# Kernel tuning notes

Measured on AMD Instinct MI355X. Metric: run time of the kernel, lower is better.

Reference implementation:

```python
import jax, jax.numpy as jnp
import numpy as np

N_E = 4096
E_DIM = 64
BETA = 0.25


def setup_inputs() -> dict:
    key = jax.random.key(0)
    k1, k2 = jax.random.split(key)
    z = jax.random.normal(k1, (16, E_DIM, 32, 32), dtype=jnp.float32)
    embedding = jax.random.normal(k2, (N_E, E_DIM), dtype=jnp.float32)
    return {"z": z, "embedding": embedding}


def reference(z, embedding):
    # b c h w -> b h w c
    zc = jnp.transpose(z, (0, 2, 3, 1))  # [B,H,W,C]
    B, H, W, C = zc.shape
    zf = zc.reshape(-1, C)  # [N, C]

    # Squared Euclidean distances (argmin is identical to cdist p=2 argmin)
    # d2[n,e] = |z|^2 - 2 z.e + |e|^2
    d2 = (
        jnp.sum(zf * zf, axis=1, keepdims=True)
        - 2.0 * (zf @ embedding.T)
        + jnp.sum(embedding * embedding, axis=1)[None, :]
    )  # [N, n_e]
    idx = jnp.argmin(d2, axis=1)  # [N]

    z_q = embedding[idx].reshape(B, H, W, C)

    # dist_p == 2 losses
    loss_d1 = jnp.mean((jax.lax.stop_gradient(z_q) - zc) ** 2)
    loss_d2 = jnp.mean((z_q - jax.lax.stop_gradient(zc)) ** 2)
    loss = BETA * loss_d1 + loss_d2

    # Straight-through estimator
    z_q = zc + jax.lax.stop_gradient(z_q - zc)

    indices = idx.reshape(B, H, W)
    z_q = jnp.transpose(z_q, (0, 3, 1, 2))  # b h w c -> b c h w
    return z_q, loss, indices
```

## Files before the change

### kernel.cpp

```cpp
#include <hip/hip_runtime.h>

typedef float f32x4 __attribute__((ext_vector_type(4)));
typedef short bf16x8 __attribute__((ext_vector_type(8)));

#define HW_ 1024
#define NE_ 4096
#define CHW_ 65536
#define ZQ_SIZE 1048576
#define LOSS_OFF ZQ_SIZE
#define IDX_OFF (ZQ_SIZE + 1)
#define LOSS_SCALE (1.25f / 1048576.f)
#define EPS_GAP 0.125f

union FragU { unsigned u[4]; bf16x8 v; };

__device__ __forceinline__ void split8(const float* v, FragU& hi, FragU& lo) {
#pragma unroll
    for (int p = 0; p < 4; p++) {
        float a = v[2 * p], b = v[2 * p + 1];
        unsigned ua = __float_as_uint(a), ub = __float_as_uint(b);
        hi.u[p] = (ua >> 16) | (ub & 0xFFFF0000u);
        float la = a - __uint_as_float(ua & 0xFFFF0000u);
        float lb = b - __uint_as_float(ub & 0xFFFF0000u);
        lo.u[p] = (__float_as_uint(la) >> 16) | (__float_as_uint(lb) & 0xFFFF0000u);
    }
}

__global__ void vq_prep(const float* __restrict__ emb, const float* __restrict__ z,
                        float* __restrict__ h_e, float* __restrict__ h_z,
                        unsigned* __restrict__ k1, unsigned* __restrict__ k2,
                        float* __restrict__ out) {
    int t = blockIdx.x * 256 + threadIdx.x;
    if (t < NE_) {
        const float4* er = (const float4*)(emb + (size_t)t * 64);
        float s = 0.f;
#pragma unroll
        for (int k = 0; k < 16; k++) {
            float4 e4 = er[k];
            s = fmaf(e4.x, e4.x, s); s = fmaf(e4.y, e4.y, s);
            s = fmaf(e4.z, e4.z, s); s = fmaf(e4.w, e4.w, s);
        }
        h_e[t] = 0.5f * s;
    } else {
        int n = t - NE_;
        int b = n >> 10, hw = n & 1023;
        const float* zp = z + (size_t)b * CHW_ + hw;
        float s = 0.f;
#pragma unroll
        for (int c = 0; c < 64; c++) { float v = zp[c * HW_]; s = fmaf(v, v, s); }
        h_z[n] = 0.5f * s;
        k1[n] = 0xFFFFFFFFu;
        k2[n] = 0xFFFFFFFFu;
        if (n == 0) out[LOSS_OFF] = 0.f;
    }
}

__global__ __launch_bounds__(256, 2) void vq_mfma(
        const float* __restrict__ z, const float* __restrict__ emb,
        const float* __restrict__ h_e, const float* __restrict__ h_z,
        unsigned* __restrict__ k1, unsigned* __restrict__ k2) {
    const int tid = threadIdx.x;
    const int lane = tid & 63;
    const int wave = tid >> 6;
    const int lrow = lane & 15;
    const int lgrp = lane >> 4;
    const int ecb = blockIdx.x & 7;
    const int rgb = blockIdx.x >> 3;

    const int ebase = ecb * 512 + wave * 128;
    const int c0 = lgrp * 8;

    FragU aeh[8][2], ael[8][2];
    float4 he4[8];
#pragma unroll
    for (int i = 0; i < 8; i++) {
        int eI = ebase + i * 16 + lrow;
        const float* ep = emb + (size_t)eI * 64;
#pragma unroll
        for (int s = 0; s < 2; s++) {
            float ev[8];
            const float4* e4p = (const float4*)(ep + s * 32 + c0);
            float4 ea = e4p[0], eb = e4p[1];
            ev[0] = -ea.x; ev[1] = -ea.y; ev[2] = -ea.z; ev[3] = -ea.w;
            ev[4] = -eb.x; ev[5] = -eb.y; ev[6] = -eb.z; ev[7] = -eb.w;
            split8(ev, aeh[i][s], ael[i][s]);
        }
        he4[i] = *(const float4*)(h_e + ebase + i * 16 + lgrp * 4);
    }

    for (int rt = 0; rt < 16; rt++) {
        const int rowbase = rgb * 256 + rt * 16;
        const int b = rowbase >> 10;
        const int hw = (rowbase & 1023) + lrow;
        const float* zc = z + (size_t)b * CHW_ + hw;

        float zr[16];
#pragma unroll
        for (int s = 0; s < 2; s++)
#pragma unroll
            for (int j = 0; j < 8; j++)
                zr[s * 8 + j] = zc[(s * 32 + c0 + j) * HW_];

        FragU bzh[2], bzl[2];
        split8(zr, bzh[0], bzl[0]);
        split8(zr + 8, bzh[1], bzl[1]);

        const float hz = h_z[rowbase + lrow];
        unsigned s1k = 0xFFFFFFFFu, s2k = 0xFFFFFFFFu;

#pragma unroll
        for (int i = 0; i < 8; i++) {
            f32x4 acc;
            acc[0] = he4[i].x + hz; acc[1] = he4[i].y + hz;
            acc[2] = he4[i].z + hz; acc[3] = he4[i].w + hz;
            acc = __builtin_amdgcn_mfma_f32_16x16x32_bf16(aeh[i][0].v, bzh[0].v, acc, 0, 0, 0);
            acc = __builtin_amdgcn_mfma_f32_16x16x32_bf16(aeh[i][1].v, bzh[1].v, acc, 0, 0, 0);
            acc = __builtin_amdgcn_mfma_f32_16x16x32_bf16(ael[i][0].v, bzh[0].v, acc, 0, 0, 0);
            acc = __builtin_amdgcn_mfma_f32_16x16x32_bf16(ael[i][1].v, bzh[1].v, acc, 0, 0, 0);
            acc = __builtin_amdgcn_mfma_f32_16x16x32_bf16(aeh[i][0].v, bzl[0].v, acc, 0, 0, 0);
            acc = __builtin_amdgcn_mfma_f32_16x16x32_bf16(aeh[i][1].v, bzl[1].v, acc, 0, 0, 0);

            const unsigned eb12 = (unsigned)(ebase + i * 16 + lgrp * 4);
#pragma unroll
            for (int r = 0; r < 4; r++) {
                float sc = fmaxf(acc[r], 0.f);
                unsigned key = (__float_as_uint(sc) & 0xFFFFF000u) | (eb12 + r);
                unsigned t2 = (s1k > key) ? s1k : key;
                s2k = (s2k < t2) ? s2k : t2;
                s1k = (s1k < key) ? s1k : key;
            }
        }

#pragma unroll
        for (int off = 16; off <= 32; off += 16) {
            unsigned o1 = (unsigned)__shfl_xor((int)s1k, off);
            unsigned o2 = (unsigned)__shfl_xor((int)s2k, off);
            unsigned t2 = (s1k > o1) ? s1k : o1;
            unsigned m2 = (s2k < o2) ? s2k : o2;
            s2k = (m2 < t2) ? m2 : t2;
            s1k = (s1k < o1) ? s1k : o1;
        }

        if (lane < 16) {
            const int n = rowbase + lane;
            unsigned old = atomicMin(&k1[n], s1k);
            unsigned disp = (old > s1k) ? old : s1k;
            atomicMin(&k2[n], disp);
            atomicMin(&k2[n], s2k);
        }
    }
}

__global__ __launch_bounds__(64) void vq_final(
        const float* __restrict__ z, const float* __restrict__ emb,
        const unsigned* __restrict__ k1v, const unsigned* __restrict__ k2v,
        float* __restrict__ out) {
    int n = blockIdx.x * 64 + threadIdx.x;
    unsigned key1 = k1v[n];
    unsigned key2 = k2v[n];
    int idx = (int)(key1 & 0xFFFu);
    float s1 = __uint_as_float(key1 & 0xFFFFF000u);
    float s2 = __uint_as_float(key2 & 0xFFFFF000u);

    int b = n >> 10, hw = n & 1023;
    const float* zp = z + (size_t)b * CHW_ + hw;

    if (s2 - s1 < EPS_GAP) {
        int i2 = (int)(key2 & 0xFFFu);
        const float* ea = emb + (size_t)idx * 64;
        const float* eb = emb + (size_t)i2 * 64;
        double da = 0.0, db = 0.0;
#pragma unroll 8
        for (int c = 0; c < 64; c++) {
            double zv = (double)zp[c * HW_];
            double xa = (double)ea[c] - zv;
            double xb = (double)eb[c] - zv;
            da = fma(xa, xa, da);
            db = fma(xb, xb, db);
        }
        if (db < da || (db == da && i2 < idx)) idx = i2;
    }

    const float* er = emb + (size_t)idx * 64;
    float* zq = out + (size_t)b * CHW_ + hw;
    float lsum = 0.f;
#pragma unroll
    for (int c = 0; c < 64; c++) {
        float e = er[c];
        float d = e - zp[c * HW_];
        zq[c * HW_] = e;
        lsum = fmaf(d, d, lsum);
    }
    out[IDX_OFF + n] = (float)idx;

#pragma unroll
    for (int off = 32; off; off >>= 1) lsum += __shfl_down(lsum, off);
    if ((threadIdx.x & 63) == 0) atomicAdd(&out[LOSS_OFF], lsum * LOSS_SCALE);
}

extern "C" void kernel_launch(void* const* d_in, const int* in_sizes, int n_in,
                              void* d_out, int out_size, void* d_ws, size_t ws_size,
                              hipStream_t stream) {
    const float* z   = (const float*)d_in[0];
    const float* emb = (const float*)d_in[1];
    float* out = (float*)d_out;
    char* ws = (char*)d_ws;

    float* h_e  = (float*)ws;
    float* h_z  = (float*)(ws + 16384);
    unsigned* k1 = (unsigned*)(ws + 16384 + 65536);
    unsigned* k2 = (unsigned*)(ws + 16384 + 65536 + 65536);

    vq_prep <<<80, 256, 0, stream>>>(emb, z, h_e, h_z, k1, k2, out);
    vq_mfma <<<512, 256, 0, stream>>>(z, emb, h_e, h_z, k1, k2);
    vq_final<<<256, 64, 0, stream>>>(z, emb, k1, k2, out);
}
```

Baseline: 58.92 us.

## Pre-split z into bf16 fragment buffer, halve codebook chunk per block, widen final kernel

Adds a kernel that splits z into hi/lo bf16 MFMA fragments once and stores them contiguously, so the main kernel reads four 16-byte vectors instead of strided scalar loads and re-splitting for every codebook chunk. The main kernel now handles 256 codes per block with 1024 blocks and a higher occupancy bound, lowering register pressure. The final kernel spreads each row's 64 channels across 4 threads, with shuffle reductions for the tie-break distances. The cost is an extra launch plus a round trip of the fragment buffer through memory, and twice as many atomic updates on the per-row keys.

Result: slower. 68.67 us (+16.6%).

```diff
diff --git a/kernel.cpp b/kernel.cpp
--- a/kernel.cpp
+++ b/kernel.cpp
@@ -55,8 +55,28 @@
     }
 }
 
-__global__ __launch_bounds__(256, 2) void vq_mfma(
-        const float* __restrict__ z, const float* __restrict__ emb,
+__global__ __launch_bounds__(256) void vq_zsplit(const float* __restrict__ z,
+                                                 char* __restrict__ zfrag) {
+    int u = blockIdx.x * 256 + threadIdx.x;
+    int l = u & 63;
+    int s = (u >> 6) & 1;
+    int t = u >> 7;
+    int n = t * 16 + (l & 15);
+    int b = n >> 10, hw = n & 1023;
+    int c0 = s * 32 + (l >> 4) * 8;
+    const float* zp = z + (size_t)b * CHW_ + hw;
+    float v[8];
+#pragma unroll
+    for (int j = 0; j < 8; j++) v[j] = zp[(c0 + j) * HW_];
+    FragU hi, lo;
+    split8(v, hi, lo);
+    char* base = zfrag + (size_t)t * 4096 + l * 16;
+    *(FragU*)(base + s * 1024) = hi;
+    *(FragU*)(base + (2 + s) * 1024) = lo;
+}
+
+__global__ __launch_bounds__(256, 4) void vq_mfma(
+        const char* __restrict__ zfrag, const float* __restrict__ emb,
         const float* __restrict__ h_e, const float* __restrict__ h_z,
         unsigned* __restrict__ k1, unsigned* __restrict__ k2) {
     const int tid = threadIdx.x;
@@ -64,16 +84,16 @@
     const int wave = tid >> 6;
     const int lrow = lane & 15;
     const int lgrp = lane >> 4;
-    const int ecb = blockIdx.x & 7;
-    const int rgb = blockIdx.x >> 3;
-
-    const int ebase = ecb * 512 + wave * 128;
+    const int ecb = blockIdx.x & 15;
+    const int rgb = blockIdx.x >> 4;
+
+    const int ebase = ecb * 256 + wave * 64;
     const int c0 = lgrp * 8;
 
-    FragU aeh[8][2], ael[8][2];
-    float4 he4[8];
-#pragma unroll
-    for (int i = 0; i < 8; i++) {
+    FragU aeh[4][2], ael[4][2];
+    float4 he4[4];
+#pragma unroll
+    for (int i = 0; i < 4; i++) {
         int eI = ebase + i * 16 + lrow;
         const float* ep = emb + (size_t)eI * 64;
 #pragma unroll
@@ -90,35 +110,26 @@
 
     for (int rt = 0; rt < 16; rt++) {
         const int rowbase = rgb * 256 + rt * 16;
-        const int b = rowbase >> 10;
-        const int hw = (rowbase & 1023) + lrow;
-        const float* zc = z + (size_t)b * CHW_ + hw;
-
-        float zr[16];
-#pragma unroll
-        for (int s = 0; s < 2; s++)
-#pragma unroll
-            for (int j = 0; j < 8; j++)
-                zr[s * 8 + j] = zc[(s * 32 + c0 + j) * HW_];
-
-        FragU bzh[2], bzl[2];
-        split8(zr, bzh[0], bzl[0]);
-        split8(zr + 8, bzh[1], bzl[1]);
-
+        const char* fb = zfrag + (size_t)(rgb * 16 + rt) * 4096 + lane * 16;
+        bf16x8 bzh0 = *(const bf16x8*)(fb);
+        bf16x8 bzh1 = *(const bf16x8*)(fb + 1024);
+        bf16x8 bzl0 = *(const bf16x8*)(fb + 2048);
+        bf16x8 bzl1 = *(const bf16x8*)(fb + 3072);
         const float hz = h_z[rowbase + lrow];
+
         unsigned s1k = 0xFFFFFFFFu, s2k = 0xFFFFFFFFu;
 
 #pragma unroll
-        for (int i = 0; i < 8; i++) {
+        for (int i = 0; i < 4; i++) {
             f32x4 acc;
             acc[0] = he4[i].x + hz; acc[1] = he4[i].y + hz;
             acc[2] = he4[i].z + hz; acc[3] = he4[i].w + hz;
-            acc = __builtin_amdgcn_mfma_f32_16x16x32_bf16(aeh[i][0].v, bzh[0].v, acc, 0, 0, 0);
-            acc = __builtin_amdgcn_mfma_f32_16x16x32_bf16(aeh[i][1].v, bzh[1].v, acc, 0, 0, 0);
-            acc = __builtin_amdgcn_mfma_f32_16x16x32_bf16(ael[i][0].v, bzh[0].v, acc, 0, 0, 0);
-            acc = __builtin_amdgcn_mfma_f32_16x16x32_bf16(ael[i][1].v, bzh[1].v, acc, 0, 0, 0);
-            acc = __builtin_amdgcn_mfma_f32_16x16x32_bf16(aeh[i][0].v, bzl[0].v, acc, 0, 0, 0);
-            acc = __builtin_amdgcn_mfma_f32_16x16x32_bf16(aeh[i][1].v, bzl[1].v, acc, 0, 0, 0);
+            acc = __builtin_amdgcn_mfma_f32_16x16x32_bf16(aeh[i][0].v, bzh0, acc, 0, 0, 0);
+            acc = __builtin_amdgcn_mfma_f32_16x16x32_bf16(aeh[i][1].v, bzh1, acc, 0, 0, 0);
+            acc = __builtin_amdgcn_mfma_f32_16x16x32_bf16(ael[i][0].v, bzh0, acc, 0, 0, 0);
+            acc = __builtin_amdgcn_mfma_f32_16x16x32_bf16(ael[i][1].v, bzh1, acc, 0, 0, 0);
+            acc = __builtin_amdgcn_mfma_f32_16x16x32_bf16(aeh[i][0].v, bzl0, acc, 0, 0, 0);
+            acc = __builtin_amdgcn_mfma_f32_16x16x32_bf16(aeh[i][1].v, bzl1, acc, 0, 0, 0);
 
             const unsigned eb12 = (unsigned)(ebase + i * 16 + lgrp * 4);
 #pragma unroll
@@ -151,11 +162,13 @@
     }
 }
 
-__global__ __launch_bounds__(64) void vq_final(
+__global__ __launch_bounds__(256) void vq_final(
         const float* __restrict__ z, const float* __restrict__ emb,
         const unsigned* __restrict__ k1v, const unsigned* __restrict__ k2v,
         float* __restrict__ out) {
-    int n = blockIdx.x * 64 + threadIdx.x;
+    int t = blockIdx.x * 256 + threadIdx.x;
+    int n = t >> 2;
+    int q = t & 3;
     unsigned key1 = k1v[n];
     unsigned key2 = k2v[n];
     int idx = (int)(key1 & 0xFFFu);
@@ -164,34 +177,40 @@
 
     int b = n >> 10, hw = n & 1023;
     const float* zp = z + (size_t)b * CHW_ + hw;
+    const int cq = q * 16;
 
     if (s2 - s1 < EPS_GAP) {
         int i2 = (int)(key2 & 0xFFFu);
-        const float* ea = emb + (size_t)idx * 64;
-        const float* eb = emb + (size_t)i2 * 64;
+        const float* ea = emb + (size_t)idx * 64 + cq;
+        const float* eb = emb + (size_t)i2 * 64 + cq;
         double da = 0.0, db = 0.0;
-#pragma unroll 8
-        for (int c = 0; c < 64; c++) {
-            double zv = (double)zp[c * HW_];
-            double xa = (double)ea[c] - zv;
-            double xb = (double)eb[c] - zv;
+#pragma unroll
+        for (int j = 0; j < 16; j++) {
+            double zv = (double)zp[(cq + j) * HW_];
+            double xa = (double)ea[j] - zv;
+            double xb = (double)eb[j] - zv;
             da = fma(xa, xa, da);
             db = fma(xb, xb, db);
         }
+#pragma unroll
+        for (int off = 1; off <= 2; off <<= 1) {
+            da += __shfl_xor(da, off);
+            db += __shfl_xor(db, off);
+        }
         if (db < da || (db == da && i2 < idx)) idx = i2;
     }
 
-    const float* er = emb + (size_t)idx * 64;
+    const float* er = emb + (size_t)idx * 64 + cq;
     float* zq = out + (size_t)b * CHW_ + hw;
     float lsum = 0.f;
 #pragma unroll
-    for (int c = 0; c < 64; c++) {
-        float e = er[c];
-        float d = e - zp[c * HW_];
-        zq[c * HW_] = e;
+    for (int j = 0; j < 16; j++) {
+        float e = er[j];
+        float d = e - zp[(cq + j) * HW_];
+        zq[(cq + j) * HW_] = e;
         lsum = fmaf(d, d, lsum);
     }
-    out[IDX_OFF + n] = (float)idx;
+    if (q == 0) out[IDX_OFF + n] = (float)idx;
 
 #pragma unroll
     for (int off = 32; off; off >>= 1) lsum += __shfl_down(lsum, off);
@@ -206,12 +225,14 @@
     float* out = (float*)d_out;
     char* ws = (char*)d_ws;
 
-    float* h_e  = (float*)ws;
-    float* h_z  = (float*)(ws + 16384);
-    unsigned* k1 = (unsigned*)(ws + 16384 + 65536);
-    unsigned* k2 = (unsigned*)(ws + 16384 + 65536 + 65536);
-
-    vq_prep <<<80, 256, 0, stream>>>(emb, z, h_e, h_z, k1, k2, out);
-    vq_mfma <<<512, 256, 0, stream>>>(z, emb, h_e, h_z, k1, k2);
-    vq_final<<<256, 64, 0, stream>>>(z, emb, k1, k2, out);
-}
+    float* h_e   = (float*)ws;
+    float* h_z   = (float*)(ws + 16384);
+    unsigned* k1 = (unsigned*)(ws + 81920);
+    unsigned* k2 = (unsigned*)(ws + 147456);
+    char* zfrag  = ws + 212992;
+
+    vq_prep  <<<80, 256, 0, stream>>>(emb, z, h_e, h_z, k1, k2, out);
+    vq_zsplit<<<512, 256, 0, stream>>>(z, zfrag);
+    vq_mfma  <<<1024, 256, 0, stream>>>(zfrag, emb, h_e, h_z, k1, k2);
+    vq_final <<<256, 256, 0, stream>>>(z, emb, k1, k2, out);
+}
```
